# Kernel tuning notes

Measured on AMD Instinct MI355X. Metric: run time of the kernel, lower is better.

The kernel has to match this reference:

```python
import jax, jax.numpy as jnp
import numpy as np

B, N, F = 64, 512, 30          # batch, pf candidates, raw features
NDIM0, NDIM = 2, 4             # coord dims: layer0 uses 2, rest use n_dim_gnn=4
NOUT, NLAYERS = 64, 5          # GNN layer width / count
NDENSE = 128
BN_EPS = 1e-3                  # keras BatchNormalization default epsilon


def setup_inputs() -> dict:
    key = jax.random.key(0)
    ks = jax.random.split(key, 20)
    xx = jax.random.normal(ks[0], (B, N, F), jnp.float32)
    # validity mask: first L_b candidates valid
    lengths = jax.random.randint(ks[1], (B,), N // 4, N + 1)
    valid = (jnp.arange(N)[None, :] < lengths[:, None]).astype(jnp.float32)
    pt = jax.random.randint(ks[2], (B, N), 0, 8).astype(jnp.float32)
    pvq = jax.random.randint(ks[3], (B, N), 0, 8).astype(jnp.float32)
    fpv = jax.random.randint(ks[4], (B, N), 0, 4).astype(jnp.float32)
    xx = xx.at[:, :, 0].set(valid).at[:, :, 27].set(pt).at[:, :, 28].set(pvq).at[:, :, 29].set(fpv)
    g = lambda k, s, sc=0.05: jax.random.normal(k, s, jnp.float32) * sc
    d_in0 = 33  # 2+2+2 embeddings + 27 float features
    return {
        "xx": xx,
        "emb1": g(ks[5], (8, 2), 0.5),
        "emb2": g(ks[6], (8, 2), 0.5),
        "emb3": g(ks[7], (4, 2), 0.5),
        "A0": g(ks[8], ((d_in0 + 1) * 2 - 1, NOUT)),   # [67,64]
        "b0": g(ks[9], (NOUT,)),
        "A_rest": g(ks[10], (NLAYERS - 1, (NOUT + 1) * 2 - 1, NOUT)),  # [4,129,64]
        "b_rest": g(ks[11], (NLAYERS - 1, NOUT)),
        "bn_gamma": jnp.ones((NLAYERS, NOUT), jnp.float32),
        "bn_beta": jnp.zeros((NLAYERS, NOUT), jnp.float32),
        "dW0": g(ks[12], (N * NOUT, NDENSE), 0.01),
        "db0": g(ks[13], (NDENSE,)),
        "dW1": g(ks[14], (NDENSE, NDENSE)),
        "db1": g(ks[15], (NDENSE,)),
        "dbn_gamma": jnp.ones((2, NDENSE), jnp.float32),
        "dbn_beta": jnp.zeros((2, NDENSE), jnp.float32),
        "W2": g(ks[16], (NDENSE, 2)),
        "b2": g(ks[17], (2,)),
    }


def _bn(x, g, b):
    # inference BatchNorm with moving_mean=0, moving_var=1 (initial stats)
    return g * x * (1.0 / jnp.sqrt(1.0 + BN_EPS)) + b


def _gnn_layer(x, mask, n_dim, A, b):
    # x: [B,N,Fin], mask: [B,N]. Original builds [B,N,N,Fin+1] via tile/reshape;
    # algebraically the reduction over senders i factorizes:
    #   ss_feat[b,j] = x[b,j] * mask[b,j] * sum_i exp(-10*d_ij)
    #   ss_last[b,j] = mask[b,j] * sum_i d_ij * exp(-10*d_ij)
    c = x[..., -n_dim:]
    diff = c[:, :, None, :] - c[:, None, :, :]      # [B,N,N,n_dim]
    dist = jnp.sum(diff * diff, axis=-1)            # [B,N,N] squared distance
    w = jnp.exp(-10.0 * dist)
    S = jnp.sum(w, axis=1)                          # [B,N] per receiver j
    T = jnp.sum(dist * w, axis=1)                   # [B,N]
    ss_feat = x * (mask * S)[..., None] - x         # subtract concat(x, 0)
    ss_last = (mask * T)[..., None]
    xcat = jnp.concatenate([x, ss_feat, ss_last], axis=-1)  # [B,N,2*Fin+1]
    return (xcat @ A + b) * mask[..., None]


def _forward(xx, emb1, emb2, emb3, A0, b0, A_rest, b_rest, bn_gamma, bn_beta,
             dW0, db0, dW1, db1, dbn_gamma, dbn_beta, W2, b2):
    mask = xx[:, :, 0]
    e1 = emb1[jnp.abs(xx[:, :, 27]).astype(jnp.int32)]
    e2 = emb2[jnp.abs(xx[:, :, 28]).astype(jnp.int32)]
    e3 = emb3[jnp.abs(xx[:, :, 29]).astype(jnp.int32)]
    x = jnp.concatenate([e1, e2, e3, xx[:, :, :27]], axis=-1)  # [B,N,33]
    x = jnp.tanh(_bn(_gnn_layer(x, mask, NDIM0, A0, b0), bn_gamma[0], bn_beta[0]))
    for k in range(NLAYERS - 1):
        x = _gnn_layer(x, mask, NDIM, A_rest[k], b_rest[k])
        x = jnp.tanh(_bn(x, bn_gamma[k + 1], bn_beta[k + 1]))
    x = x.reshape(B, N * NOUT)
    x = jax.nn.sigmoid(_bn(x @ dW0 + db0, dbn_gamma[0], dbn_beta[0]))
    x = jax.nn.sigmoid(_bn(x @ dW1 + db1, dbn_gamma[1], dbn_beta[1]))
    x = x @ W2 + b2                                  # [B,2]
    # mode == 'dm': concat zeros on the right
    return jnp.concatenate([x, jnp.zeros((B, 2), x.dtype)], axis=1)


def reference(xx, emb1, emb2, emb3, A0, b0, A_rest, b_rest, bn_gamma, bn_beta,
              dW0, db0, dW1, db1, dbn_gamma, dbn_beta, W2, b2):
    return _forward(xx, emb1, emb2, emb3, A0, b0, A_rest, b_rest, bn_gamma, bn_beta,
                    dW0, db0, dW1, db1, dbn_gamma, dbn_beta, W2, b2)
```

## Files before the change

### kernel.cpp

```cpp
#include <hip/hip_runtime.h>
#include <math.h>

#define B_ 64
#define N_ 512
#define NOUT_ 64
#define R_ (B_*N_)
#define INV_S 0.9995003746877732f

template<int KP, int XS, int LAYER0>
__global__ __launch_bounds__(256, 4) void gnn_layer(
    const float* __restrict__ xx, const float* __restrict__ xin,
    const float* __restrict__ A, int K,
    const float* __restrict__ bias, const float* __restrict__ gamma,
    const float* __restrict__ beta,
    const float* __restrict__ emb1, const float* __restrict__ emb2,
    const float* __restrict__ emb3, float* __restrict__ xout)
{
  __shared__ float4 cl[512];
  __shared__ float alo[KP*64];
  __shared__ float ahi[KP*64];
  __shared__ float xl[64*XS];
  __shared__ float spart[256], tpart[256];
  __shared__ float scl[64], tcl[64], ml[64];

  int tid = threadIdx.x;
  int jc = blockIdx.x;
  int b  = blockIdx.y;
  int rbase = b*N_;
  int jloc  = jc*64;

  if constexpr (LAYER0){
    for (int i = tid; i < 512; i += 256){
      const float* row = xx + (size_t)(rbase+i)*30;
      cl[i] = make_float4(row[25], row[26], 0.f, 0.f);
    }
  } else {
    for (int i = tid; i < 512; i += 256){
      cl[i] = *(const float4*)&xin[(size_t)(rbase+i)*64 + 60];
    }
  }

  if constexpr (KP == 64){
    const float4* A4 = (const float4*)A;
    float4* alo4 = (float4*)alo;
    float4* ahi4 = (float4*)ahi;
    for (int idx = tid; idx < 1024; idx += 256){
      alo4[idx] = A4[idx];
      ahi4[idx] = A4[1024 + idx];
    }
  } else {
    for (int idx = tid; idx < KP*64; idx += 256){
      int f = idx >> 6;
      alo[idx] = (f < K) ? A[idx] : 0.f;
      ahi[idx] = (f < K) ? A[(size_t)K*64 + idx] : 0.f;
    }
  }

  if constexpr (LAYER0){
    if (tid < 64){
      int r = rbase + jloc + tid;
      const float* row = xx + (size_t)r*30;
      float v[30];
#pragma unroll
      for (int i=0;i<30;i++) v[i] = row[i];
      int i1 = (int)fabsf(v[27]);
      int i2 = (int)fabsf(v[28]);
      int i3 = (int)fabsf(v[29]);
      float* o = &xl[tid*XS];
      o[0]=emb1[i1*2+0]; o[1]=emb1[i1*2+1];
      o[2]=emb2[i2*2+0]; o[3]=emb2[i2*2+1];
      o[4]=emb3[i3*2+0]; o[5]=emb3[i3*2+1];
#pragma unroll
      for (int i=0;i<27;i++) o[6+i] = v[i];
      o[33]=0.f; o[34]=0.f; o[35]=0.f;
      ml[tid] = v[0];
    }
  } else {
    for (int idx = tid; idx < 1024; idx += 256){
      int jj = idx >> 4, fq = idx & 15;
      *(float4*)&xl[jj*XS + fq*4] =
          *(const float4*)&xin[(size_t)(rbase+jloc+jj)*64 + fq*4];
    }
    if (tid < 64) ml[tid] = xx[(size_t)(rbase+jloc+tid)*30];
  }
  __syncthreads();

  {
    int jj = tid & 63, q = tid >> 6;
    float4 cj = cl[jloc + jj];
    float Ss = 0.f, Ts = 0.f;
    int base = q*128;
#pragma unroll 8
    for (int i=0;i<128;i++){
      float4 ci = cl[base+i];
      float d0 = cj.x-ci.x, d1 = cj.y-ci.y, d2 = cj.z-ci.z, d3 = cj.w-ci.w;
      float dist = d0*d0 + d1*d1 + d2*d2 + d3*d3;
      float w = __expf(-10.f*dist);
      Ss += w;
      Ts += dist*w;
    }
    spart[tid] = Ss;
    tpart[tid] = Ts;
  }
  __syncthreads();
  if (tid < 64){
    float S = spart[tid] + spart[tid+64] + spart[tid+128] + spart[tid+192];
    float T = tpart[tid] + tpart[tid+64] + tpart[tid+128] + tpart[tid+192];
    float m = ml[tid];
    scl[tid] = m*S - 1.f;
    tcl[tid] = m*T;
  }
  __syncthreads();

  int o0 = (tid & 15)*4, r0 = (tid >> 4)*4;
  float4 acc1[4], acc2[4];
#pragma unroll
  for (int rr=0;rr<4;rr++){
    acc1[rr] = make_float4(0.f,0.f,0.f,0.f);
    acc2[rr] = make_float4(0.f,0.f,0.f,0.f);
  }
#pragma unroll 1
  for (int kc = 0; kc < KP; kc += 4){
    float4 a1[4], a2[4], xv[4];
#pragma unroll
    for (int u=0;u<4;u++){
      a1[u] = *(const float4*)&alo[(kc+u)*64 + o0];
      a2[u] = *(const float4*)&ahi[(kc+u)*64 + o0];
    }
#pragma unroll
    for (int rr=0;rr<4;rr++)
      xv[rr] = *(const float4*)&xl[(r0+rr)*XS + kc];
#pragma unroll
    for (int u=0;u<4;u++){
#pragma unroll
      for (int rr=0;rr<4;rr++){
        float xu = ((const float*)&xv[rr])[u];
        acc1[rr].x = fmaf(xu, a1[u].x, acc1[rr].x);
        acc1[rr].y = fmaf(xu, a1[u].y, acc1[rr].y);
        acc1[rr].z = fmaf(xu, a1[u].z, acc1[rr].z);
        acc1[rr].w = fmaf(xu, a1[u].w, acc1[rr].w);
        acc2[rr].x = fmaf(xu, a2[u].x, acc2[rr].x);
        acc2[rr].y = fmaf(xu, a2[u].y, acc2[rr].y);
        acc2[rr].z = fmaf(xu, a2[u].z, acc2[rr].z);
        acc2[rr].w = fmaf(xu, a2[u].w, acc2[rr].w);
      }
    }
  }

  float4 alast = *(const float4*)&A[(size_t)2*K*64 + o0];
  float4 bo = *(const float4*)&bias[o0];
  float4 go = *(const float4*)&gamma[o0];
  float4 be = *(const float4*)&beta[o0];
#pragma unroll
  for (int rr=0;rr<4;rr++){
    int r = rbase + jloc + r0 + rr;
    float sc = scl[r0+rr], tc = tcl[r0+rr], m = ml[r0+rr];
    float4 v;
    v.x = (acc1[rr].x + sc*acc2[rr].x + tc*alast.x + bo.x)*m;
    v.y = (acc1[rr].y + sc*acc2[rr].y + tc*alast.y + bo.y)*m;
    v.z = (acc1[rr].z + sc*acc2[rr].z + tc*alast.z + bo.z)*m;
    v.w = (acc1[rr].w + sc*acc2[rr].w + tc*alast.w + bo.w)*m;
    float4 t;
    t.x = tanhf(go.x*(v.x*INV_S) + be.x);
    t.y = tanhf(go.y*(v.y*INV_S) + be.y);
    t.z = tanhf(go.z*(v.z*INV_S) + be.z);
    t.w = tanhf(go.w*(v.w*INV_S) + be.w);
    *(float4*)&xout[(size_t)r*64 + o0] = t;
  }
}

__global__ __launch_bounds__(256) void dense0_partial(
    const float* __restrict__ X, const float* __restrict__ W,
    float* __restrict__ partial)
{
  __shared__ float xt[64*32];
  __shared__ float wt[32*128];
  int tid = threadIdx.x;
  int k0 = blockIdx.x*128;
  int og = (tid & 15)*8;
  int rg = (tid >> 4)*4;
  float acc[4][8];
#pragma unroll
  for (int a=0;a<4;a++)
#pragma unroll
    for (int u=0;u<8;u++) acc[a][u]=0.f;
  for (int kt = 0; kt < 128; kt += 32){
    __syncthreads();
    for (int idx = tid; idx < 512; idx += 256){
      int r = idx >> 3, kq = idx & 7;
      *(float4*)&xt[r*32 + kq*4] =
          *(const float4*)&X[(size_t)r*32768 + k0 + kt + kq*4];
    }
    {
      const float4* Wc = (const float4*)&W[(size_t)(k0+kt)*128];
      float4* wt4 = (float4*)wt;
      for (int idx = tid; idx < 1024; idx += 256) wt4[idx] = Wc[idx];
    }
    __syncthreads();
#pragma unroll 4
    for (int k=0;k<32;k++){
      float4 w0 = *(const float4*)&wt[k*128 + og];
      float4 w1 = *(const float4*)&wt[k*128 + og + 4];
      float xs[4];
#pragma unroll
      for (int rr=0;rr<4;rr++) xs[rr] = xt[(rg+rr)*32 + k];
#pragma unroll
      for (int rr=0;rr<4;rr++){
        acc[rr][0] = fmaf(xs[rr], w0.x, acc[rr][0]);
        acc[rr][1] = fmaf(xs[rr], w0.y, acc[rr][1]);
        acc[rr][2] = fmaf(xs[rr], w0.z, acc[rr][2]);
        acc[rr][3] = fmaf(xs[rr], w0.w, acc[rr][3]);
        acc[rr][4] = fmaf(xs[rr], w1.x, acc[rr][4]);
        acc[rr][5] = fmaf(xs[rr], w1.y, acc[rr][5]);
        acc[rr][6] = fmaf(xs[rr], w1.z, acc[rr][6]);
        acc[rr][7] = fmaf(xs[rr], w1.w, acc[rr][7]);
      }
    }
  }
  float* pb = partial + (size_t)blockIdx.x*8192;
#pragma unroll
  for (int rr=0;rr<4;rr++){
    *(float4*)&pb[(rg+rr)*128 + og]     = *(float4*)&acc[rr][0];
    *(float4*)&pb[(rg+rr)*128 + og + 4] = *(float4*)&acc[rr][4];
  }
}

__global__ __launch_bounds__(256) void dense_head(
    const float* __restrict__ partial,
    const float* __restrict__ db0, const float* __restrict__ dg0,
    const float* __restrict__ dbb0,
    const float* __restrict__ dW1, const float* __restrict__ db1,
    const float* __restrict__ dg1, const float* __restrict__ dbb1,
    const float* __restrict__ W2, const float* __restrict__ b2,
    float* __restrict__ out)
{
  __shared__ float sred[256];
  __shared__ float h[128];
  __shared__ float red0[128], red1[128];
  int tid = threadIdx.x;
  int b = blockIdx.x;
  int o = tid & 127, ph = tid >> 7;
  float s = 0.f;
#pragma unroll 16
  for (int p = ph*128; p < ph*128+128; p++)
    s += partial[(size_t)p*8192 + b*128 + o];
  sred[tid] = s;
  __syncthreads();
  if (tid < 128){
    float sum = sred[tid] + sred[tid+128];
    float v = dg0[tid]*((sum + db0[tid])*INV_S) + dbb0[tid];
    h[tid] = 1.f/(1.f + __expf(-v));
  }
  __syncthreads();
  if (tid < 128){
    float acc = 0.f;
#pragma unroll 8
    for (int k=0;k<128;k++) acc = fmaf(h[k], dW1[k*128 + tid], acc);
    float v = dg1[tid]*((acc + db1[tid])*INV_S) + dbb1[tid];
    float h1 = 1.f/(1.f + __expf(-v));
    red0[tid] = h1 * W2[tid*2+0];
    red1[tid] = h1 * W2[tid*2+1];
  }
  __syncthreads();
  for (int st=64; st>0; st>>=1){
    if (tid < st){ red0[tid] += red0[tid+st]; red1[tid] += red1[tid+st]; }
    __syncthreads();
  }
  if (tid == 0){
    out[b*4+0] = red0[0] + b2[0];
    out[b*4+1] = red1[0] + b2[1];
    out[b*4+2] = 0.f;
    out[b*4+3] = 0.f;
  }
}

extern "C" void kernel_launch(void* const* d_in, const int* in_sizes, int n_in,
                              void* d_out, int out_size, void* d_ws, size_t ws_size,
                              hipStream_t stream)
{
  const float* xx   = (const float*)d_in[0];
  const float* emb1 = (const float*)d_in[1];
  const float* emb2 = (const float*)d_in[2];
  const float* emb3 = (const float*)d_in[3];
  const float* A0   = (const float*)d_in[4];
  const float* b0   = (const float*)d_in[5];
  const float* Ar   = (const float*)d_in[6];
  const float* br   = (const float*)d_in[7];
  const float* bng  = (const float*)d_in[8];
  const float* bnb  = (const float*)d_in[9];
  const float* dW0  = (const float*)d_in[10];
  const float* db0  = (const float*)d_in[11];
  const float* dW1  = (const float*)d_in[12];
  const float* db1  = (const float*)d_in[13];
  const float* dbg  = (const float*)d_in[14];
  const float* dbb  = (const float*)d_in[15];
  const float* W2   = (const float*)d_in[16];
  const float* b2   = (const float*)d_in[17];

  float* ws = (float*)d_ws;
  float* xA      = ws;
  float* xB      = xA + (size_t)R_*64;
  float* partial = xB + (size_t)R_*64;

  dim3 lgrid(8, 64);
  gnn_layer<36,44,1><<<lgrid, 256, 0, stream>>>(
      xx, nullptr, A0, 33, b0, bng, bnb, emb1, emb2, emb3, xA);
  float* bufs[2] = {xA, xB};
  int curi = 0;
  for (int k=0;k<4;k++){
    const float* cur = bufs[curi];
    float* nxt = bufs[1-curi];
    gnn_layer<64,68,0><<<lgrid, 256, 0, stream>>>(
        xx, cur, Ar + (size_t)k*129*64, 64, br + k*64,
        bng + (k+1)*64, bnb + (k+1)*64, emb1, emb2, emb3, nxt);
    curi ^= 1;
  }
  const float* x5 = bufs[curi];

  dense0_partial<<<256, 256, 0, stream>>>(x5, dW0, partial);
  dense_head<<<B_, 256, 0, stream>>>(partial, db0, dbg, dbb,
                                     dW1, db1, dbg + 128, dbb + 128,
                                     W2, b2, (float*)d_out);
}
```

Baseline: 246.6 us.

## Fuse all GNN layers and dense head into one cooperative persistent kernel

Replaces the seven separate launches (five GNN layers, the dense partial GEMM and the dense head) with one cooperative kernel of 256 blocks, using grid.sync between stages and a shared-memory union reused across phases. Each block now processes two 64-row chunks per layer, and the dense stage loads 64-wide k tiles. This removes per-launch overhead and inter-kernel gaps. In exchange, each layer runs with half as many blocks and serialized sub-chunks, layer 0 pads K from 36 to 64, and the grid-wide barriers add cost.

```diff
diff --git a/kernel.cpp b/kernel.cpp
--- a/kernel.cpp
+++ b/kernel.cpp
@@ -1,276 +1,292 @@
 #include <hip/hip_runtime.h>
+#include <hip/hip_cooperative_groups.h>
 #include <math.h>
+
+namespace cg = cooperative_groups;
 
 #define B_ 64
 #define N_ 512
-#define NOUT_ 64
 #define R_ (B_*N_)
 #define INV_S 0.9995003746877732f
 
-template<int KP, int XS, int LAYER0>
-__global__ __launch_bounds__(256, 4) void gnn_layer(
-    const float* __restrict__ xx, const float* __restrict__ xin,
-    const float* __restrict__ A, int K,
-    const float* __restrict__ bias, const float* __restrict__ gamma,
-    const float* __restrict__ beta,
-    const float* __restrict__ emb1, const float* __restrict__ emb2,
-    const float* __restrict__ emb3, float* __restrict__ xout)
+struct FusedArgs {
+  const float* xx;
+  const float* emb1; const float* emb2; const float* emb3;
+  const float* A0;  const float* b0;
+  const float* Ar;  const float* br;
+  const float* bng; const float* bnb;
+  const float* dW0; const float* db0;
+  const float* dW1; const float* db1;
+  const float* dbg; const float* dbb;
+  const float* W2;  const float* b2;
+  float* xA; float* xB; float* partial;
+  float* out;
+};
+
+__global__ __launch_bounds__(256, 4) void gnn_fused(FusedArgs a)
 {
-  __shared__ float4 cl[512];
-  __shared__ float alo[KP*64];
-  __shared__ float ahi[KP*64];
-  __shared__ float xl[64*XS];
-  __shared__ float spart[256], tpart[256];
+  __shared__ union {
+    struct {
+      float4 cl[512];
+      float alo[64*64];
+      float ahi[64*64];
+      float xl[64*68];
+      float spart[256], tpart[256];
+    } lay;
+    struct {
+      float xt[64*68];
+      float wt[64*128];
+    } den;
+    struct {
+      float sred[256]; float h[128]; float red0[128]; float red1[128];
+    } head;
+  } u;
   __shared__ float scl[64], tcl[64], ml[64];
 
+  cg::grid_group grid = cg::this_grid();
   int tid = threadIdx.x;
-  int jc = blockIdx.x;
-  int b  = blockIdx.y;
+  int bid = blockIdx.x;
+  int b = bid >> 2, q4 = bid & 3;
   int rbase = b*N_;
-  int jloc  = jc*64;
-
-  if constexpr (LAYER0){
-    for (int i = tid; i < 512; i += 256){
-      const float* row = xx + (size_t)(rbase+i)*30;
-      cl[i] = make_float4(row[25], row[26], 0.f, 0.f);
-    }
-  } else {
-    for (int i = tid; i < 512; i += 256){
-      cl[i] = *(const float4*)&xin[(size_t)(rbase+i)*64 + 60];
-    }
+
+  for (int L = 0; L < 5; L++){
+    const float* A    = (L==0) ? a.A0 : (a.Ar + (size_t)(L-1)*129*64);
+    const float* bias = (L==0) ? a.b0 : (a.br + (L-1)*64);
+    const float* gam  = a.bng + L*64;
+    const float* bet  = a.bnb + L*64;
+    int K = (L==0) ? 33 : 64;
+    const float* xin  = (L&1) ? a.xA : a.xB;
+    float* xout       = (L&1) ? a.xB : a.xA;
+
+    if (L == 0){
+      for (int i = tid; i < 512; i += 256){
+        const float* row = a.xx + (size_t)(rbase+i)*30;
+        u.lay.cl[i] = make_float4(row[25], row[26], 0.f, 0.f);
+      }
+    } else {
+      for (int i = tid; i < 512; i += 256)
+        u.lay.cl[i] = *(const float4*)&xin[(size_t)(rbase+i)*64 + 60];
+    }
+
+    for (int idx = tid; idx < 4096; idx += 256){
+      int f = idx >> 6;
+      u.lay.alo[idx] = (f < K) ? A[idx] : 0.f;
+      u.lay.ahi[idx] = (f < K) ? A[(size_t)K*64 + idx] : 0.f;
+    }
+
+    for (int sub = 0; sub < 2; sub++){
+      int jloc = (q4*2 + sub)*64;
+      __syncthreads();
+
+      if (L == 0){
+        if (tid < 64){
+          int r = rbase + jloc + tid;
+          const float* row = a.xx + (size_t)r*30;
+          float v[30];
+#pragma unroll
+          for (int i=0;i<30;i++) v[i] = row[i];
+          int i1 = (int)fabsf(v[27]);
+          int i2 = (int)fabsf(v[28]);
+          int i3 = (int)fabsf(v[29]);
+          float* o = &u.lay.xl[tid*68];
+          o[0]=a.emb1[i1*2+0]; o[1]=a.emb1[i1*2+1];
+          o[2]=a.emb2[i2*2+0]; o[3]=a.emb2[i2*2+1];
+          o[4]=a.emb3[i3*2+0]; o[5]=a.emb3[i3*2+1];
+#pragma unroll
+          for (int i=0;i<27;i++) o[6+i] = v[i];
+#pragma unroll
+          for (int i=33;i<64;i++) o[i] = 0.f;
+          ml[tid] = v[0];
+        }
+      } else {
+        for (int idx = tid; idx < 1024; idx += 256){
+          int jj = idx >> 4, fq = idx & 15;
+          *(float4*)&u.lay.xl[jj*68 + fq*4] =
+              *(const float4*)&xin[(size_t)(rbase+jloc+jj)*64 + fq*4];
+        }
+        if (tid < 64) ml[tid] = a.xx[(size_t)(rbase+jloc+tid)*30];
+      }
+      __syncthreads();
+
+      {
+        int jj = tid & 63, q = tid >> 6;
+        float4 cj = u.lay.cl[jloc + jj];
+        float Ss = 0.f, Ts = 0.f;
+        int base = q*128;
+#pragma unroll 8
+        for (int i=0;i<128;i++){
+          float4 ci = u.lay.cl[base+i];
+          float d0 = cj.x-ci.x, d1 = cj.y-ci.y, d2 = cj.z-ci.z, d3 = cj.w-ci.w;
+          float dist = d0*d0 + d1*d1 + d2*d2 + d3*d3;
+          float w = __expf(-10.f*dist);
+          Ss += w;
+          Ts += dist*w;
+        }
+        u.lay.spart[tid] = Ss;
+        u.lay.tpart[tid] = Ts;
+      }
+      __syncthreads();
+      if (tid < 64){
+        float S = u.lay.spart[tid] + u.lay.spart[tid+64]
+                + u.lay.spart[tid+128] + u.lay.spart[tid+192];
+        float T = u.lay.tpart[tid] + u.lay.tpart[tid+64]
+                + u.lay.tpart[tid+128] + u.lay.tpart[tid+192];
+        float m = ml[tid];
+        scl[tid] = m*S - 1.f;
+        tcl[tid] = m*T;
+      }
+      __syncthreads();
+
+      int o0 = (tid & 15)*4, r0 = (tid >> 4)*4;
+      float4 acc1[4], acc2[4];
+#pragma unroll
+      for (int rr=0;rr<4;rr++){
+        acc1[rr] = make_float4(0.f,0.f,0.f,0.f);
+        acc2[rr] = make_float4(0.f,0.f,0.f,0.f);
+      }
+#pragma unroll 1
+      for (int kc = 0; kc < 64; kc += 4){
+        float4 a1[4], a2[4], xv[4];
+#pragma unroll
+        for (int uu=0;uu<4;uu++){
+          a1[uu] = *(const float4*)&u.lay.alo[(kc+uu)*64 + o0];
+          a2[uu] = *(const float4*)&u.lay.ahi[(kc+uu)*64 + o0];
+        }
+#pragma unroll
+        for (int rr=0;rr<4;rr++)
+          xv[rr] = *(const float4*)&u.lay.xl[(r0+rr)*68 + kc];
+#pragma unroll
+        for (int uu=0;uu<4;uu++){
+#pragma unroll
+          for (int rr=0;rr<4;rr++){
+            float xu = ((const float*)&xv[rr])[uu];
+            acc1[rr].x = fmaf(xu, a1[uu].x, acc1[rr].x);
+            acc1[rr].y = fmaf(xu, a1[uu].y, acc1[rr].y);
+            acc1[rr].z = fmaf(xu, a1[uu].z, acc1[rr].z);
+            acc1[rr].w = fmaf(xu, a1[uu].w, acc1[rr].w);
+            acc2[rr].x = fmaf(xu, a2[uu].x, acc2[rr].x);
+            acc2[rr].y = fmaf(xu, a2[uu].y, acc2[rr].y);
+            acc2[rr].z = fmaf(xu, a2[uu].z, acc2[rr].z);
+            acc2[rr].w = fmaf(xu, a2[uu].w, acc2[rr].w);
+          }
+        }
+      }
+
+      float4 alast = *(const float4*)&A[(size_t)2*K*64 + o0];
+      float4 bo = *(const float4*)&bias[o0];
+      float4 go = *(const float4*)&gam[o0];
+      float4 be = *(const float4*)&bet[o0];
+#pragma unroll
+      for (int rr=0;rr<4;rr++){
+        int r = rbase + jloc + r0 + rr;
+        float sc = scl[r0+rr], tc = tcl[r0+rr], m = ml[r0+rr];
+        float4 v;
+        v.x = (acc1[rr].x + sc*acc2[rr].x + tc*alast.x + bo.x)*m;
+        v.y = (acc1[rr].y + sc*acc2[rr].y + tc*alast.y + bo.y)*m;
+        v.z = (acc1[rr].z + sc*acc2[rr].z + tc*alast.z + bo.z)*m;
+        v.w = (acc1[rr].w + sc*acc2[rr].w + tc*alast.w + bo.w)*m;
+        float4 t;
+        t.x = tanhf(go.x*(v.x*INV_S) + be.x);
+        t.y = tanhf(go.y*(v.y*INV_S) + be.y);
+        t.z = tanhf(go.z*(v.z*INV_S) + be.z);
+        t.w = tanhf(go.w*(v.w*INV_S) + be.w);
+        *(float4*)&xout[(size_t)r*64 + o0] = t;
+      }
+    }
+    __threadfence();
+    grid.sync();
   }
 
-  if constexpr (KP == 64){
-    const float4* A4 = (const float4*)A;
-    float4* alo4 = (float4*)alo;
-    float4* ahi4 = (float4*)ahi;
-    for (int idx = tid; idx < 1024; idx += 256){
-      alo4[idx] = A4[idx];
-      ahi4[idx] = A4[1024 + idx];
-    }
-  } else {
-    for (int idx = tid; idx < KP*64; idx += 256){
-      int f = idx >> 6;
-      alo[idx] = (f < K) ? A[idx] : 0.f;
-      ahi[idx] = (f < K) ? A[(size_t)K*64 + idx] : 0.f;
-    }
+  {
+    int k0 = bid*128;
+    const float* X = a.xA;
+    int og = (tid & 15)*8, rg = (tid >> 4)*4;
+    float acc[4][8];
+#pragma unroll
+    for (int rr=0;rr<4;rr++)
+#pragma unroll
+      for (int uu=0;uu<8;uu++) acc[rr][uu]=0.f;
+    for (int kt = 0; kt < 128; kt += 64){
+      __syncthreads();
+      for (int idx = tid; idx < 1024; idx += 256){
+        int r = idx >> 4, kq = idx & 15;
+        *(float4*)&u.den.xt[r*68 + kq*4] =
+            *(const float4*)&X[(size_t)r*32768 + k0 + kt + kq*4];
+      }
+      {
+        const float4* Wc = (const float4*)&a.dW0[(size_t)(k0+kt)*128];
+        float4* wt4 = (float4*)u.den.wt;
+        for (int idx = tid; idx < 2048; idx += 256) wt4[idx] = Wc[idx];
+      }
+      __syncthreads();
+#pragma unroll 4
+      for (int k=0;k<64;k++){
+        float4 w0 = *(const float4*)&u.den.wt[k*128 + og];
+        float4 w1 = *(const float4*)&u.den.wt[k*128 + og + 4];
+        float xs[4];
+#pragma unroll
+        for (int rr=0;rr<4;rr++) xs[rr] = u.den.xt[(rg+rr)*68 + k];
+#pragma unroll
+        for (int rr=0;rr<4;rr++){
+          acc[rr][0] = fmaf(xs[rr], w0.x, acc[rr][0]);
+          acc[rr][1] = fmaf(xs[rr], w0.y, acc[rr][1]);
+          acc[rr][2] = fmaf(xs[rr], w0.z, acc[rr][2]);
+          acc[rr][3] = fmaf(xs[rr], w0.w, acc[rr][3]);
+          acc[rr][4] = fmaf(xs[rr], w1.x, acc[rr][4]);
+          acc[rr][5] = fmaf(xs[rr], w1.y, acc[rr][5]);
+          acc[rr][6] = fmaf(xs[rr], w1.z, acc[rr][6]);
+          acc[rr][7] = fmaf(xs[rr], w1.w, acc[rr][7]);
+        }
+      }
+    }
+    float* pb = a.partial + (size_t)bid*8192;
+#pragma unroll
+    for (int rr=0;rr<4;rr++){
+      *(float4*)&pb[(rg+rr)*128 + og]     = *(float4*)&acc[rr][0];
+      *(float4*)&pb[(rg+rr)*128 + og + 4] = *(float4*)&acc[rr][4];
+    }
+    __threadfence();
   }
-
-  if constexpr (LAYER0){
-    if (tid < 64){
-      int r = rbase + jloc + tid;
-      const float* row = xx + (size_t)r*30;
-      float v[30];
-#pragma unroll
-      for (int i=0;i<30;i++) v[i] = row[i];
-      int i1 = (int)fabsf(v[27]);
-      int i2 = (int)fabsf(v[28]);
-      int i3 = (int)fabsf(v[29]);
-      float* o = &xl[tid*XS];
-      o[0]=emb1[i1*2+0]; o[1]=emb1[i1*2+1];
-      o[2]=emb2[i2*2+0]; o[3]=emb2[i2*2+1];
-      o[4]=emb3[i3*2+0]; o[5]=emb3[i3*2+1];
-#pragma unroll
-      for (int i=0;i<27;i++) o[6+i] = v[i];
-      o[33]=0.f; o[34]=0.f; o[35]=0.f;
-      ml[tid] = v[0];
-    }
-  } else {
-    for (int idx = tid; idx < 1024; idx += 256){
-      int jj = idx >> 4, fq = idx & 15;
-      *(float4*)&xl[jj*XS + fq*4] =
-          *(const float4*)&xin[(size_t)(rbase+jloc+jj)*64 + fq*4];
-    }
-    if (tid < 64) ml[tid] = xx[(size_t)(rbase+jloc+tid)*30];
-  }
-  __syncthreads();
-
-  {
-    int jj = tid & 63, q = tid >> 6;
-    float4 cj = cl[jloc + jj];
-    float Ss = 0.f, Ts = 0.f;
-    int base = q*128;
+  grid.sync();
+
+  if (bid < 64){
+    int bb = bid;
+    int o = tid & 127, ph = tid >> 7;
+    float s = 0.f;
+#pragma unroll 16
+    for (int p = ph*128; p < ph*128+128; p++)
+      s += a.partial[(size_t)p*8192 + bb*128 + o];
+    u.head.sred[tid] = s;
+    __syncthreads();
+    if (tid < 128){
+      float sum = u.head.sred[tid] + u.head.sred[tid+128];
+      float v = a.dbg[tid]*((sum + a.db0[tid])*INV_S) + a.dbb[tid];
+      u.head.h[tid] = 1.f/(1.f + __expf(-v));
+    }
+    __syncthreads();
+    if (tid < 128){
+      float acc = 0.f;
 #pragma unroll 8
-    for (int i=0;i<128;i++){
-      float4 ci = cl[base+i];
-      float d0 = cj.x-ci.x, d1 = cj.y-ci.y, d2 = cj.z-ci.z, d3 = cj.w-ci.w;
-      float dist = d0*d0 + d1*d1 + d2*d2 + d3*d3;
-      float w = __expf(-10.f*dist);
-      Ss += w;
-      Ts += dist*w;
-    }
-    spart[tid] = Ss;
-    tpart[tid] = Ts;
-  }
-  __syncthreads();
-  if (tid < 64){
-    float S = spart[tid] + spart[tid+64] + spart[tid+128] + spart[tid+192];
-    float T = tpart[tid] + tpart[tid+64] + tpart[tid+128] + tpart[tid+192];
-    float m = ml[tid];
-    scl[tid] = m*S - 1.f;
-    tcl[tid] = m*T;
-  }
-  __syncthreads();
-
-  int o0 = (tid & 15)*4, r0 = (tid >> 4)*4;
-  float4 acc1[4], acc2[4];
-#pragma unroll
-  for (int rr=0;rr<4;rr++){
-    acc1[rr] = make_float4(0.f,0.f,0.f,0.f);
-    acc2[rr] = make_float4(0.f,0.f,0.f,0.f);
-  }
-#pragma unroll 1
-  for (int kc = 0; kc < KP; kc += 4){
-    float4 a1[4], a2[4], xv[4];
-#pragma unroll
-    for (int u=0;u<4;u++){
-      a1[u] = *(const float4*)&alo[(kc+u)*64 + o0];
-      a2[u] = *(const float4*)&ahi[(kc+u)*64 + o0];
-    }
-#pragma unroll
-    for (int rr=0;rr<4;rr++)
-      xv[rr] = *(const float4*)&xl[(r0+rr)*XS + kc];
-#pragma unroll
-    for (int u=0;u<4;u++){
-#pragma unroll
-      for (int rr=0;rr<4;rr++){
-        float xu = ((const float*)&xv[rr])[u];
-        acc1[rr].x = fmaf(xu, a1[u].x, acc1[rr].x);
-        acc1[rr].y = fmaf(xu, a1[u].y, acc1[rr].y);
-        acc1[rr].z = fmaf(xu, a1[u].z, acc1[rr].z);
-        acc1[rr].w = fmaf(xu, a1[u].w, acc1[rr].w);
-        acc2[rr].x = fmaf(xu, a2[u].x, acc2[rr].x);
-        acc2[rr].y = fmaf(xu, a2[u].y, acc2[rr].y);
-        acc2[rr].z = fmaf(xu, a2[u].z, acc2[rr].z);
-        acc2[rr].w = fmaf(xu, a2[u].w, acc2[rr].w);
-      }
-    }
-  }
-
-  float4 alast = *(const float4*)&A[(size_t)2*K*64 + o0];
-  float4 bo = *(const float4*)&bias[o0];
-  float4 go = *(const float4*)&gamma[o0];
-  float4 be = *(const float4*)&beta[o0];
-#pragma unroll
-  for (int rr=0;rr<4;rr++){
-    int r = rbase + jloc + r0 + rr;
-    float sc = scl[r0+rr], tc = tcl[r0+rr], m = ml[r0+rr];
-    float4 v;
-    v.x = (acc1[rr].x + sc*acc2[rr].x + tc*alast.x + bo.x)*m;
-    v.y = (acc1[rr].y + sc*acc2[rr].y + tc*alast.y + bo.y)*m;
-    v.z = (acc1[rr].z + sc*acc2[rr].z + tc*alast.z + bo.z)*m;
-    v.w = (acc1[rr].w + sc*acc2[rr].w + tc*alast.w + bo.w)*m;
-    float4 t;
-    t.x = tanhf(go.x*(v.x*INV_S) + be.x);
-    t.y = tanhf(go.y*(v.y*INV_S) + be.y);
-    t.z = tanhf(go.z*(v.z*INV_S) + be.z);
-    t.w = tanhf(go.w*(v.w*INV_S) + be.w);
-    *(float4*)&xout[(size_t)r*64 + o0] = t;
-  }
-}
-
-__global__ __launch_bounds__(256) void dense0_partial(
-    const float* __restrict__ X, const float* __restrict__ W,
-    float* __restrict__ partial)
-{
-  __shared__ float xt[64*32];
-  __shared__ float wt[32*128];
-  int tid = threadIdx.x;
-  int k0 = blockIdx.x*128;
-  int og = (tid & 15)*8;
-  int rg = (tid >> 4)*4;
-  float acc[4][8];
-#pragma unroll
-  for (int a=0;a<4;a++)
-#pragma unroll
-    for (int u=0;u<8;u++) acc[a][u]=0.f;
-  for (int kt = 0; kt < 128; kt += 32){
+      for (int k=0;k<128;k++) acc = fmaf(u.head.h[k], a.dW1[k*128 + tid], acc);
+      float v = a.dbg[128+tid]*((acc + a.db1[tid])*INV_S) + a.dbb[128+tid];
+      float h1 = 1.f/(1.f + __expf(-v));
+      u.head.red0[tid] = h1 * a.W2[tid*2+0];
+      u.head.red1[tid] = h1 * a.W2[tid*2+1];
+    }
     __syncthreads();
-    for (int idx = tid; idx < 512; idx += 256){
-      int r = idx >> 3, kq = idx & 7;
-      *(float4*)&xt[r*32 + kq*4] =
-          *(const float4*)&X[(size_t)r*32768 + k0 + kt + kq*4];
-    }
-    {
-      const float4* Wc = (const float4*)&W[(size_t)(k0+kt)*128];
-      float4* wt4 = (float4*)wt;
-      for (int idx = tid; idx < 1024; idx += 256) wt4[idx] = Wc[idx];
-    }
-    __syncthreads();
-#pragma unroll 4
-    for (int k=0;k<32;k++){
-      float4 w0 = *(const float4*)&wt[k*128 + og];
-      float4 w1 = *(const float4*)&wt[k*128 + og + 4];
-      float xs[4];
-#pragma unroll
-      for (int rr=0;rr<4;rr++) xs[rr] = xt[(rg+rr)*32 + k];
-#pragma unroll
-      for (int rr=0;rr<4;rr++){
-        acc[rr][0] = fmaf(xs[rr], w0.x, acc[rr][0]);
-        acc[rr][1] = fmaf(xs[rr], w0.y, acc[rr][1]);
-        acc[rr][2] = fmaf(xs[rr], w0.z, acc[rr][2]);
-        acc[rr][3] = fmaf(xs[rr], w0.w, acc[rr][3]);
-        acc[rr][4] = fmaf(xs[rr], w1.x, acc[rr][4]);
-        acc[rr][5] = fmaf(xs[rr], w1.y, acc[rr][5]);
-        acc[rr][6] = fmaf(xs[rr], w1.z, acc[rr][6]);
-        acc[rr][7] = fmaf(xs[rr], w1.w, acc[rr][7]);
-      }
-    }
-  }
-  float* pb = partial + (size_t)blockIdx.x*8192;
-#pragma unroll
-  for (int rr=0;rr<4;rr++){
-    *(float4*)&pb[(rg+rr)*128 + og]     = *(float4*)&acc[rr][0];
-    *(float4*)&pb[(rg+rr)*128 + og + 4] = *(float4*)&acc[rr][4];
-  }
-}
-
-__global__ __launch_bounds__(256) void dense_head(
-    const float* __restrict__ partial,
-    const float* __restrict__ db0, const float* __restrict__ dg0,
-    const float* __restrict__ dbb0,
-    const float* __restrict__ dW1, const float* __restrict__ db1,
-    const float* __restrict__ dg1, const float* __restrict__ dbb1,
-    const float* __restrict__ W2, const float* __restrict__ b2,
-    float* __restrict__ out)
-{
-  __shared__ float sred[256];
-  __shared__ float h[128];
-  __shared__ float red0[128], red1[128];
-  int tid = threadIdx.x;
-  int b = blockIdx.x;
-  int o = tid & 127, ph = tid >> 7;
-  float s = 0.f;
-#pragma unroll 16
-  for (int p = ph*128; p < ph*128+128; p++)
-    s += partial[(size_t)p*8192 + b*128 + o];
-  sred[tid] = s;
-  __syncthreads();
-  if (tid < 128){
-    float sum = sred[tid] + sred[tid+128];
-    float v = dg0[tid]*((sum + db0[tid])*INV_S) + dbb0[tid];
-    h[tid] = 1.f/(1.f + __expf(-v));
-  }
-  __syncthreads();
-  if (tid < 128){
-    float acc = 0.f;
-#pragma unroll 8
-    for (int k=0;k<128;k++) acc = fmaf(h[k], dW1[k*128 + tid], acc);
-    float v = dg1[tid]*((acc + db1[tid])*INV_S) + dbb1[tid];
-    float h1 = 1.f/(1.f + __expf(-v));
-    red0[tid] = h1 * W2[tid*2+0];
-    red1[tid] = h1 * W2[tid*2+1];
-  }
-  __syncthreads();
-  for (int st=64; st>0; st>>=1){
-    if (tid < st){ red0[tid] += red0[tid+st]; red1[tid] += red1[tid+st]; }
-    __syncthreads();
-  }
-  if (tid == 0){
-    out[b*4+0] = red0[0] + b2[0];
-    out[b*4+1] = red1[0] + b2[1];
-    out[b*4+2] = 0.f;
-    out[b*4+3] = 0.f;
+    for (int st=64; st>0; st>>=1){
+      if (tid < st){
+        u.head.red0[tid] += u.head.red0[tid+st];
+        u.head.red1[tid] += u.head.red1[tid+st];
+      }
+      __syncthreads();
+    }
+    if (tid == 0){
+      a.out[bb*4+0] = u.head.red0[0] + a.b2[0];
+      a.out[bb*4+1] = u.head.red1[0] + a.b2[1];
+      a.out[bb*4+2] = 0.f;
+      a.out[bb*4+3] = 0.f;
+    }
   }
 }
 
@@ -278,47 +294,32 @@
                               void* d_out, int out_size, void* d_ws, size_t ws_size,
                               hipStream_t stream)
 {
-  const float* xx   = (const float*)d_in[0];
-  const float* emb1 = (const float*)d_in[1];
-  const float* emb2 = (const float*)d_in[2];
-  const float* emb3 = (const float*)d_in[3];
-  const float* A0   = (const float*)d_in[4];
-  const float* b0   = (const float*)d_in[5];
-  const float* Ar   = (const float*)d_in[6];
-  const float* br   = (const float*)d_in[7];
-  const float* bng  = (const float*)d_in[8];
-  const float* bnb  = (const float*)d_in[9];
-  const float* dW0  = (const float*)d_in[10];
-  const float* db0  = (const float*)d_in[11];
-  const float* dW1  = (const float*)d_in[12];
-  const float* db1  = (const float*)d_in[13];
-  const float* dbg  = (const float*)d_in[14];
-  const float* dbb  = (const float*)d_in[15];
-  const float* W2   = (const float*)d_in[16];
-  const float* b2   = (const float*)d_in[17];
-
   float* ws = (float*)d_ws;
-  float* xA      = ws;
-  float* xB      = xA + (size_t)R_*64;
-  float* partial = xB + (size_t)R_*64;
-
-  dim3 lgrid(8, 64);
-  gnn_layer<36,44,1><<<lgrid, 256, 0, stream>>>(
-      xx, nullptr, A0, 33, b0, bng, bnb, emb1, emb2, emb3, xA);
-  float* bufs[2] = {xA, xB};
-  int curi = 0;
-  for (int k=0;k<4;k++){
-    const float* cur = bufs[curi];
-    float* nxt = bufs[1-curi];
-    gnn_layer<64,68,0><<<lgrid, 256, 0, stream>>>(
-        xx, cur, Ar + (size_t)k*129*64, 64, br + k*64,
-        bng + (k+1)*64, bnb + (k+1)*64, emb1, emb2, emb3, nxt);
-    curi ^= 1;
-  }
-  const float* x5 = bufs[curi];
-
-  dense0_partial<<<256, 256, 0, stream>>>(x5, dW0, partial);
-  dense_head<<<B_, 256, 0, stream>>>(partial, db0, dbg, dbb,
-                                     dW1, db1, dbg + 128, dbb + 128,
-                                     W2, b2, (float*)d_out);
+  FusedArgs fa;
+  fa.xx   = (const float*)d_in[0];
+  fa.emb1 = (const float*)d_in[1];
+  fa.emb2 = (const float*)d_in[2];
+  fa.emb3 = (const float*)d_in[3];
+  fa.A0   = (const float*)d_in[4];
+  fa.b0   = (const float*)d_in[5];
+  fa.Ar   = (const float*)d_in[6];
+  fa.br   = (const float*)d_in[7];
+  fa.bng  = (const float*)d_in[8];
+  fa.bnb  = (const float*)d_in[9];
+  fa.dW0  = (const float*)d_in[10];
+  fa.db0  = (const float*)d_in[11];
+  fa.dW1  = (const float*)d_in[12];
+  fa.db1  = (const float*)d_in[13];
+  fa.dbg  = (const float*)d_in[14];
+  fa.dbb  = (const float*)d_in[15];
+  fa.W2   = (const float*)d_in[16];
+  fa.b2   = (const float*)d_in[17];
+  fa.xA   = ws;
+  fa.xB   = fa.xA + (size_t)R_*64;
+  fa.partial = fa.xB + (size_t)R_*64;
+  fa.out  = (float*)d_out;
+
+  void* kargs[] = { &fa };
+  hipLaunchCooperativeKernel((const void*)gnn_fused, dim3(256), dim3(256),
+                             kargs, 0, stream);
 }
```

New measurement: 631.2 us. 156% more time.
